# Kernel optimization log

Hardware: AMD Instinct MI355X
Metric: run time of the kernel (lower is better)

The kernel has to match this reference:

```python
import jax, jax.numpy as jnp
import numpy as np

N = 50000   # num_nodes
E = 400000  # random edges (avg degree 8)


def setup_inputs() -> dict:
    key = jax.random.key(0)
    ks = jax.random.split(key, 12)

    def w(k, shape):
        # xavier-ish scaling
        return (jax.random.normal(k, shape, jnp.float32)
                / jnp.sqrt(jnp.float32(shape[0])))

    return {
        "node_emb": jax.random.normal(ks[0], (N, 128), jnp.float32) * 0.05,
        "edge_index": jax.random.randint(ks[1], (2, E), 0, N, dtype=jnp.int32),
        "W1": w(ks[2], (128, 512)), "b1": jnp.zeros((512,), jnp.float32),
        "W2": w(ks[3], (512, 128)), "b2": jnp.zeros((128,), jnp.float32),
        "Wres": w(ks[4], (512, 128)), "bres": jnp.zeros((128,), jnp.float32),
        "Wfc1": w(ks[5], (128, 256)), "bfc1": jnp.zeros((256,), jnp.float32),
        "Wfc2": w(ks[6], (256, 1)), "bfc2": jnp.zeros((1,), jnp.float32),
    }


def reference(node_emb, edge_index, W1, b1, W2, b2, Wres, bres,
              Wfc1, bfc1, Wfc2, bfc2):
    n = node_emb.shape[0]
    loops = jnp.arange(n, dtype=edge_index.dtype)
    # explicit add_self_loops in forward + GCNConv's internal gcn_norm self
    # loops => each node gets TWO self loops (faithful to the torch code).
    src = jnp.concatenate([edge_index[0], loops, loops])
    dst = jnp.concatenate([edge_index[1], loops, loops])

    deg = jax.ops.segment_sum(jnp.ones(src.shape, node_emb.dtype), dst,
                              num_segments=n)
    dinv = jnp.where(deg > 0, jax.lax.rsqrt(deg), 0.0)
    norm = dinv[src] * dinv[dst]  # [Etot]

    def gcn(x, W, b):
        h = x @ W                                    # [N, out]
        msg = h[src] * norm[:, None]                 # gather + scale
        agg = jax.ops.segment_sum(msg, dst, num_segments=n)  # scatter-add
        return agg + b

    x1 = jax.nn.relu(gcn(node_emb, W1, b1))   # [N, 512] (dropout = eval/id)
    x2 = jax.nn.relu(gcn(x1, W2, b2))          # [N, 128]
    x = x2 + x1 @ Wres + bres                  # residual projection
    A = jax.nn.relu(x @ Wfc1 + bfc1) @ Wfc2 + bfc2  # [N, 1]
    return (x, A)
```

## Files before the change

### kernel.cpp

```cpp
#include <hip/hip_runtime.h>


typedef unsigned short u16;
typedef short bf16x8 __attribute__((ext_vector_type(8)));
typedef unsigned short us8 __attribute__((ext_vector_type(8)));
typedef float f32x4 __attribute__((ext_vector_type(4)));

static inline int cdiv_ll(long long a, long long b) { return (int)((a + b - 1) / b); }

__device__ inline float bf2f(u16 u) {
    union { unsigned int i; float f; } v; v.i = ((unsigned int)u) << 16; return v.f;
}
__device__ inline u16 f2bf(float x) {
    union { float f; unsigned int i; } v; v.f = x;
    unsigned int r = v.i + 0x7fffu + ((v.i >> 16) & 1u);
    return (u16)(r >> 16);
}


__global__ __launch_bounds__(256) void setup_kernel(const float* __restrict__ emb,
                                                    const float* __restrict__ W1,
                                                    const float* __restrict__ W2,
                                                    const float* __restrict__ Wres,
                                                    const float* __restrict__ Wfc1,
                                                    const float* __restrict__ bfc2,
                                                    u16* __restrict__ embb,
                                                    u16* __restrict__ W1t,
                                                    u16* __restrict__ Wct,
                                                    u16* __restrict__ Wfc1t,
                                                    int* __restrict__ cnt,
                                                    float* __restrict__ Aout,
                                                    int N) {
    long long r = (long long)blockIdx.x * 256 + threadIdx.x;
    const long long nf2b = (long long)N * 32;
    if (r < nf2b) {
        float4 v = ((const float4*)emb)[r];
        uint2 o;
        o.x = (unsigned)f2bf(v.x) | ((unsigned)f2bf(v.y) << 16);
        o.y = (unsigned)f2bf(v.z) | ((unsigned)f2bf(v.w) << 16);
        ((uint2*)embb)[r] = o;
        return;
    }
    r -= nf2b;
    if (r < 512 * 128) {
        int n = (int)(r / 128), k = (int)(r % 128);
        W1t[r] = f2bf(W1[(size_t)k * 512 + n]);
        return;
    }
    r -= 512 * 128;
    if (r < 256 * 512) {
        int n = (int)(r / 512), k = (int)(r % 512);
        float v = (n < 128) ? W2[(size_t)k * 128 + n] : Wres[(size_t)k * 128 + (n - 128)];
        Wct[r] = f2bf(v);
        return;
    }
    r -= 256 * 512;
    if (r < 256 * 128) {
        int n = (int)(r / 128), k = (int)(r % 128);
        Wfc1t[r] = f2bf(Wfc1[(size_t)k * 256 + n]);
        return;
    }
    r -= 256 * 128;
    if (r < N) { cnt[(int)r] = 0; return; }
    r -= N;
    if (r < N) Aout[(int)r] = bfc2[0];
}


__global__ __launch_bounds__(256) void hist_kernel(const int* __restrict__ dst,
                                                   int* __restrict__ cnt, int E) {
    int e = blockIdx.x * 256 + threadIdx.x;
    if (e < E) atomicAdd(&cnt[dst[e]], 1);
}

__global__ __launch_bounds__(256) void scanA_kernel(const int* __restrict__ cnt,
                                                    int* __restrict__ excl,
                                                    int* __restrict__ bsum, int N) {
    __shared__ int tmp[256];
    int i = blockIdx.x * 256 + threadIdx.x;
    int v = (i < N) ? cnt[i] : 0;
    tmp[threadIdx.x] = v;
    __syncthreads();
    for (int o = 1; o < 256; o <<= 1) {
        int t = (threadIdx.x >= (unsigned)o) ? tmp[threadIdx.x - o] : 0;
        __syncthreads();
        tmp[threadIdx.x] += t;
        __syncthreads();
    }
    if (i < N) excl[i] = tmp[threadIdx.x] - v;
    if (threadIdx.x == 255) bsum[blockIdx.x] = tmp[255];
}

__global__ __launch_bounds__(256) void scanC2_kernel(const int* __restrict__ excl,
                                                     const int* __restrict__ bsum,
                                                     const int* __restrict__ cnt,
                                                     int* __restrict__ rowptr,
                                                     int* __restrict__ cursor,
                                                     float* __restrict__ dinv,
                                                     int N, int E) {
    __shared__ int tmp[256];
    int t = threadIdx.x;
    tmp[t] = (t < (int)blockIdx.x) ? bsum[t] : 0;
    __syncthreads();
    for (int o = 128; o; o >>= 1) {
        if (t < o) tmp[t] += tmp[t + o];
        __syncthreads();
    }
    int pre = tmp[0];
    int i = blockIdx.x * 256 + t;
    if (i < N) {
        int r = excl[i] + pre;
        rowptr[i] = r;
        cursor[i] = r;
        dinv[i] = rsqrtf((float)cnt[i] + 2.0f);
    }
    if (i == 0) rowptr[N] = E;
}

__global__ __launch_bounds__(256) void fill_kernel(const int* __restrict__ src,
                                                   const int* __restrict__ dst,
                                                   const float* __restrict__ dinv,
                                                   int* __restrict__ cursor,
                                                   int* __restrict__ csr_src,
                                                   float* __restrict__ csr_w, int E) {
    int e = blockIdx.x * 256 + threadIdx.x;
    if (e >= E) return;
    int s = src[e], d = dst[e];
    int idx = atomicAdd(&cursor[d], 1);
    csr_src[idx] = s;
    csr_w[idx] = dinv[s] * dinv[d];
}


#define AGG_EDGE(SR, WR)                                                       \
    {                                                                          \
        unsigned int vv = hp[(size_t)(SR) * 64 + lane];                        \
        ax = fmaf(bf2f((u16)vv), (WR), ax);                                    \
        ay = fmaf(bf2f((u16)(vv >> 16)), (WR), ay);                            \
    }

__device__ inline void agg_row(const unsigned int* __restrict__ hp,
                               const int* __restrict__ rowptr,
                               const int* __restrict__ csr_src,
                               const float* __restrict__ csr_w,
                               const float* __restrict__ dinv,
                               int wid, int lane, float& ax, float& ay) {
    float dv = dinv[wid];
    unsigned int hv = hp[(size_t)wid * 64 + lane];
    float c0 = 2.0f * dv * dv;
    ax = bf2f((u16)hv) * c0;
    ay = bf2f((u16)(hv >> 16)) * c0;
    int e = rowptr[wid], e1 = rowptr[wid + 1];
    for (; e + 7 < e1; e += 8) {
        int s0 = csr_src[e + 0], s1 = csr_src[e + 1], s2 = csr_src[e + 2], s3 = csr_src[e + 3];
        int s4 = csr_src[e + 4], s5 = csr_src[e + 5], s6 = csr_src[e + 6], s7 = csr_src[e + 7];
        float w0 = csr_w[e + 0], w1 = csr_w[e + 1], w2 = csr_w[e + 2], w3 = csr_w[e + 3];
        float w4 = csr_w[e + 4], w5 = csr_w[e + 5], w6 = csr_w[e + 6], w7 = csr_w[e + 7];
        AGG_EDGE(s0, w0); AGG_EDGE(s1, w1); AGG_EDGE(s2, w2); AGG_EDGE(s3, w3);
        AGG_EDGE(s4, w4); AGG_EDGE(s5, w5); AGG_EDGE(s6, w6); AGG_EDGE(s7, w7);
    }
    if (e + 3 < e1) {
        int s0 = csr_src[e + 0], s1 = csr_src[e + 1], s2 = csr_src[e + 2], s3 = csr_src[e + 3];
        float w0 = csr_w[e + 0], w1 = csr_w[e + 1], w2 = csr_w[e + 2], w3 = csr_w[e + 3];
        AGG_EDGE(s0, w0); AGG_EDGE(s1, w1); AGG_EDGE(s2, w2); AGG_EDGE(s3, w3);
        e += 4;
    }
    for (; e < e1; ++e) {
        int s0 = csr_src[e]; float w0 = csr_w[e];
        AGG_EDGE(s0, w0);
    }
}

__global__ __launch_bounds__(256) void aggb_kernel(const u16* __restrict__ hb,
                                                   const int* __restrict__ rowptr,
                                                   const int* __restrict__ csr_src,
                                                   const float* __restrict__ csr_w,
                                                   const float* __restrict__ dinv,
                                                   u16* __restrict__ out, int N) {
    int wid  = (blockIdx.x * blockDim.x + threadIdx.x) >> 6;
    int lane = threadIdx.x & 63;
    if (wid >= N) return;
    float ax, ay;
    agg_row((const unsigned int*)hb, rowptr, csr_src, csr_w, dinv, wid, lane, ax, ay);
    ((unsigned int*)out)[(size_t)wid * 64 + lane] =
        (unsigned)f2bf(ax) | ((unsigned)f2bf(ay) << 16);
}

__global__ __launch_bounds__(256) void aggfin_kernel(const u16* __restrict__ hb,
                                                     const int* __restrict__ rowptr,
                                                     const int* __restrict__ csr_src,
                                                     const float* __restrict__ csr_w,
                                                     const float* __restrict__ dinv,
                                                     const float* __restrict__ b2,
                                                     const float* __restrict__ bres,
                                                     float* __restrict__ xout,
                                                     u16* __restrict__ xb, int N) {
    int wid  = (blockIdx.x * blockDim.x + threadIdx.x) >> 6;
    int lane = threadIdx.x & 63;
    if (wid >= N) return;
    float ax, ay;
    agg_row((const unsigned int*)hb, rowptr, csr_src, csr_w, dinv, wid, lane, ax, ay);
    float2 bb = ((const float2*)b2)[lane];
    float2 rr = ((const float2*)bres)[lane];
    float2 hres = ((float2*)xout)[(size_t)wid * 64 + lane];
    float ox = fmaxf(ax + bb.x, 0.f) + hres.x + rr.x;
    float oy = fmaxf(ay + bb.y, 0.f) + hres.y + rr.y;
    ((float2*)xout)[(size_t)wid * 64 + lane] = make_float2(ox, oy);
    ((unsigned int*)xb)[(size_t)wid * 64 + lane] =
        (unsigned)f2bf(ox) | ((unsigned)f2bf(oy) << 16);
}


__global__ __launch_bounds__(512) void mgemm12(const u16* __restrict__ aggE,
                                               const u16* __restrict__ W1t,
                                               const u16* __restrict__ Wct,
                                               const float* __restrict__ b1,
                                               int M,
                                               u16* __restrict__ h2b,
                                               float* __restrict__ xout) {
    extern __shared__ u16 smem[];
    u16* Ag  = smem;
    u16* Ws  = Ag + 128 * 136;
    u16* X1s = Ws + 256 * 136;
    const int LD = 136;

    const int t = threadIdx.x;
    const int bm = blockIdx.x * 128;
    const int w = t >> 6, lane = t & 63;
    const int wm = w >> 2, wn = w & 3;
    const int l15 = lane & 15, lg = lane >> 4;

#pragma unroll
    for (int i = 0; i < 4; ++i) {
        int c = t + 512 * i;
        int row = c >> 4, cs = (c & 15) * 8;
        us8 v = (us8)(u16)0;
        if (bm + row < M) v = *(const us8*)(aggE + (size_t)(bm + row) * 128 + cs);
        *(us8*)&Ag[row * LD + cs] = v;
    }

    f32x4 acc2[4][4];
#pragma unroll
    for (int i = 0; i < 4; ++i)
#pragma unroll
        for (int j = 0; j < 4; ++j) acc2[i][j] = (f32x4)(0.0f);

    for (int p = 0; p < 4; ++p) {
        __syncthreads();
#pragma unroll
        for (int i = 0; i < 4; ++i) {
            int c = t + 512 * i;
            int row = c >> 4, cs = (c & 15) * 8;
            *(us8*)&Ws[row * LD + cs] =
                *(const us8*)(W1t + (size_t)(128 * p + row) * 128 + cs);
        }
        __syncthreads();

        f32x4 acc1[4][2];
#pragma unroll
        for (int i = 0; i < 4; ++i)
#pragma unroll
            for (int j = 0; j < 2; ++j) acc1[i][j] = (f32x4)(0.0f);
#pragma unroll
        for (int ks = 0; ks < 4; ++ks) {
            const int ko = 32 * ks + lg * 8;
            bf16x8 wfr[2], afr[4];
#pragma unroll
            for (int fn = 0; fn < 2; ++fn)
                wfr[fn] = *(const bf16x8*)&Ws[(32 * wn + 16 * fn + l15) * LD + ko];
#pragma unroll
            for (int fm = 0; fm < 4; ++fm)
                afr[fm] = *(const bf16x8*)&Ag[(64 * wm + 16 * fm + l15) * LD + ko];
#pragma unroll
            for (int fm = 0; fm < 4; ++fm)
#pragma unroll
                for (int fn = 0; fn < 2; ++fn)
                    acc1[fm][fn] = __builtin_amdgcn_mfma_f32_16x16x32_bf16(
                        wfr[fn], afr[fm], acc1[fm][fn], 0, 0, 0);
        }
        __syncthreads();

#pragma unroll
        for (int fm = 0; fm < 4; ++fm) {
#pragma unroll
            for (int fn = 0; fn < 2; ++fn) {
                int col1 = 32 * wn + 16 * fn + 4 * lg;
                float4 b4 = *(const float4*)&b1[128 * p + col1];
                f32x4 v = acc1[fm][fn];
                float v0 = fmaxf(v[0] + b4.x, 0.f), v1 = fmaxf(v[1] + b4.y, 0.f);
                float v2 = fmaxf(v[2] + b4.z, 0.f), v3 = fmaxf(v[3] + b4.w, 0.f);
                uint2 o;
                o.x = (unsigned)f2bf(v0) | ((unsigned)f2bf(v1) << 16);
                o.y = (unsigned)f2bf(v2) | ((unsigned)f2bf(v3) << 16);
                *(uint2*)&X1s[(64 * wm + 16 * fm + l15) * LD + col1] = o;
            }
        }
#pragma unroll
        for (int i = 0; i < 8; ++i) {
            int c = t + 512 * i;
            int row = c >> 4, cs = (c & 15) * 8;
            *(us8*)&Ws[row * LD + cs] =
                *(const us8*)(Wct + (size_t)row * 512 + 128 * p + cs);
        }
        __syncthreads();

#pragma unroll
        for (int ks = 0; ks < 4; ++ks) {
            const int ko = 32 * ks + lg * 8;
            bf16x8 wfr[4], xfr[4];
#pragma unroll
            for (int fn = 0; fn < 4; ++fn)
                wfr[fn] = *(const bf16x8*)&Ws[(64 * wn + 16 * fn + l15) * LD + ko];
#pragma unroll
            for (int fm = 0; fm < 4; ++fm)
                xfr[fm] = *(const bf16x8*)&X1s[(64 * wm + 16 * fm + l15) * LD + ko];
#pragma unroll
            for (int fm = 0; fm < 4; ++fm)
#pragma unroll
                for (int fn = 0; fn < 4; ++fn)
                    acc2[fm][fn] = __builtin_amdgcn_mfma_f32_16x16x32_bf16(
                        wfr[fn], xfr[fm], acc2[fm][fn], 0, 0, 0);
        }
    }

#pragma unroll
    for (int fm = 0; fm < 4; ++fm) {
        const int row = bm + 64 * wm + 16 * fm + l15;
        if (row >= M) continue;
#pragma unroll
        for (int fn = 0; fn < 4; ++fn) {
            const int col = 64 * wn + 16 * fn + 4 * lg;
            f32x4 v = acc2[fm][fn];
            if (col < 128) {
                uint2 o;
                o.x = (unsigned)f2bf(v[0]) | ((unsigned)f2bf(v[1]) << 16);
                o.y = (unsigned)f2bf(v[2]) | ((unsigned)f2bf(v[3]) << 16);
                *(uint2*)(h2b + (size_t)row * 128 + col) = o;
            } else {
                *(float4*)(xout + (size_t)row * 128 + (col - 128)) =
                    make_float4(v[0], v[1], v[2], v[3]);
            }
        }
    }
}


__global__ __launch_bounds__(512) void head_gemm(const u16* __restrict__ A,
                                                 const u16* __restrict__ Bt,
                                                 int M,
                                                 const float* __restrict__ bias,
                                                 const float* __restrict__ w2,
                                                 float* __restrict__ Cf) {
    __shared__ u16 As[128][72];
    __shared__ u16 Bs[256][72];
    const int t = threadIdx.x;
    const int bm = blockIdx.x * 128;
    const int w = t >> 6, lane = t & 63;
    const int wm = w >> 2, wn = w & 3;
    const int l15 = lane & 15, lg = lane >> 4;
    const int srow = t >> 3, scol = (t & 7) * 8;
    const int K = 128;

    f32x4 acc[4][4];
#pragma unroll
    for (int i = 0; i < 4; ++i)
#pragma unroll
        for (int j = 0; j < 4; ++j) acc[i][j] = (f32x4)(0.0f);

    for (int kk = 0; kk < K; kk += 64) {
#pragma unroll
        for (int i = 0; i < 2; ++i) {
            int row = srow + 64 * i;
            us8 v = (us8)(u16)0;
            if (bm + row < M)
                v = *(const us8*)(A + (size_t)(bm + row) * K + kk + scol);
            *(us8*)&As[row][scol] = v;
        }
#pragma unroll
        for (int i = 0; i < 4; ++i) {
            int row = srow + 64 * i;
            *(us8*)&Bs[row][scol] =
                *(const us8*)(Bt + (size_t)row * K + kk + scol);
        }
        __syncthreads();
#pragma unroll
        for (int ks = 0; ks < 2; ++ks) {
            const int ko = 32 * ks + lg * 8;
            bf16x8 bfr[4], afr[4];
#pragma unroll
            for (int fn = 0; fn < 4; ++fn)
                bfr[fn] = *(const bf16x8*)&Bs[64 * wn + 16 * fn + l15][ko];
#pragma unroll
            for (int fm = 0; fm < 4; ++fm)
                afr[fm] = *(const bf16x8*)&As[64 * wm + 16 * fm + l15][ko];
#pragma unroll
            for (int fm = 0; fm < 4; ++fm)
#pragma unroll
                for (int fn = 0; fn < 4; ++fn)
                    acc[fm][fn] = __builtin_amdgcn_mfma_f32_16x16x32_bf16(
                        bfr[fn], afr[fm], acc[fm][fn], 0, 0, 0);
        }
        __syncthreads();
    }

    float4 bl4[4], wl4[4];
#pragma unroll
    for (int fn = 0; fn < 4; ++fn) {
        int c = 64 * wn + 16 * fn + 4 * lg;
        bl4[fn] = *(const float4*)&bias[c];
        wl4[fn] = *(const float4*)&w2[c];
    }
#pragma unroll
    for (int fm = 0; fm < 4; ++fm) {
        float p = 0.f;
#pragma unroll
        for (int fn = 0; fn < 4; ++fn) {
            p += fmaxf(acc[fm][fn][0] + bl4[fn].x, 0.f) * wl4[fn].x;
            p += fmaxf(acc[fm][fn][1] + bl4[fn].y, 0.f) * wl4[fn].y;
            p += fmaxf(acc[fm][fn][2] + bl4[fn].z, 0.f) * wl4[fn].z;
            p += fmaxf(acc[fm][fn][3] + bl4[fn].w, 0.f) * wl4[fn].w;
        }
        p += __shfl_xor(p, 16);
        p += __shfl_xor(p, 32);
        int row = bm + 64 * wm + 16 * fm + l15;
        if (lane < 16 && row < M) atomicAdd(&Cf[row], p);
    }
}


extern "C" void kernel_launch(void* const* d_in, const int* in_sizes, int n_in,
                              void* d_out, int out_size, void* d_ws, size_t ws_size,
                              hipStream_t stream) {
    const float* emb  = (const float*)d_in[0];
    const int*   eidx = (const int*)d_in[1];
    const float* W1   = (const float*)d_in[2];
    const float* b1   = (const float*)d_in[3];
    const float* W2   = (const float*)d_in[4];
    const float* b2   = (const float*)d_in[5];
    const float* Wres = (const float*)d_in[6];
    const float* bres = (const float*)d_in[7];
    const float* Wfc1 = (const float*)d_in[8];
    const float* bfc1 = (const float*)d_in[9];
    const float* Wfc2 = (const float*)d_in[10];
    const float* bfc2 = (const float*)d_in[11];

    const int N = in_sizes[0] / 128;
    const int E = in_sizes[1] / 2;
    const int* srcv = eidx;
    const int* dstv = eidx + E;

    float* out  = (float*)d_out;
    float* xout = out;
    float* Aout = out + (size_t)N * 128;

    char* p = (char*)d_ws;
    float* dinv  = (float*)p;            p += (size_t)N * 4;
    float* csr_w = (float*)p;            p += (size_t)E * 4;
    u16*  embb   = (u16*)p;              p += (size_t)N * 128 * 2;
    u16*  aggEb  = (u16*)p;              p += (size_t)N * 128 * 2;
    u16*  h2b    = (u16*)p;              p += (size_t)N * 128 * 2;
    u16*  xb     = (u16*)p;              p += (size_t)N * 128 * 2;
    u16*  W1t    = (u16*)p;              p += (size_t)512 * 128 * 2;
    u16*  Wct    = (u16*)p;              p += (size_t)256 * 512 * 2;
    u16*  Wfc1t  = (u16*)p;              p += (size_t)256 * 128 * 2;
    int*  cnt     = (int*)p;             p += (size_t)N * 4;
    int*  excl    = (int*)p;             p += (size_t)N * 4;
    int*  rowptr  = (int*)p;             p += (size_t)(N + 1) * 4;
    int*  cursor  = (int*)p;             p += (size_t)N * 4;
    int*  bsum    = (int*)p;             p += 256 * 4;
    int*  csr_src = (int*)p;             p += (size_t)E * 4;

    const int T  = 256;
    const int nb = cdiv_ll(N, 256);

    const long long setup_work = (long long)N * 32 + 512 * 128 + 256 * 512
                               + 256 * 128 + (long long)N + (long long)N;
    setup_kernel<<<cdiv_ll(setup_work, T), T, 0, stream>>>(
        emb, W1, W2, Wres, Wfc1, bfc2, embb, W1t, Wct, Wfc1t, cnt, Aout, N);

    hist_kernel<<<cdiv_ll(E, T), T, 0, stream>>>(dstv, cnt, E);
    scanA_kernel<<<nb, T, 0, stream>>>(cnt, excl, bsum, N);
    scanC2_kernel<<<nb, T, 0, stream>>>(excl, bsum, cnt, rowptr, cursor, dinv, N, E);
    fill_kernel<<<cdiv_ll(E, T), T, 0, stream>>>(srcv, dstv, dinv, cursor, csr_src, csr_w, E);

    aggb_kernel<<<cdiv_ll((long long)N * 64, T), T, 0, stream>>>(
        embb, rowptr, csr_src, csr_w, dinv, aggEb, N);

    const size_t lds12 = (size_t)(128 * 136 + 256 * 136 + 128 * 136) * sizeof(u16);
    mgemm12<<<cdiv_ll(N, 128), 512, lds12, stream>>>(
        aggEb, W1t, Wct, b1, N, h2b, xout);

    aggfin_kernel<<<cdiv_ll((long long)N * 64, T), T, 0, stream>>>(
        h2b, rowptr, csr_src, csr_w, dinv, b2, bres, xout, xb, N);

    head_gemm<<<cdiv_ll(N, 128), 512, 0, stream>>>(
        xb, Wfc1t, N, bfc1, Wfc2, Aout);
}
```

Baseline: 178.3 us.

## Shrink mgemm12 tile to 64 rows and feed head GEMM from fp32 output

The fused two-layer GEMM now uses a 64-row tile with 4 waves. A fragments stay in registers and weight fragments are loaded straight from global memory (L2-cached) instead of being staged in LDS, so only the X1 intermediate lives in shared memory. The smaller LDS footprint should raise occupancy and remove several barriers, but weight reads are now repeated per wave from global memory. Separately, aggfin no longer writes a bf16 copy of x, and head_gemm converts the fp32 output to bf16 on load, saving one write pass at the cost of reading twice as many bytes.

```diff
diff --git a/kernel.cpp b/kernel.cpp
--- a/kernel.cpp
+++ b/kernel.cpp
@@ -193,8 +193,7 @@
                                                      const float* __restrict__ dinv,
                                                      const float* __restrict__ b2,
                                                      const float* __restrict__ bres,
-                                                     float* __restrict__ xout,
-                                                     u16* __restrict__ xb, int N) {
+                                                     float* __restrict__ xout, int N) {
     int wid  = (blockIdx.x * blockDim.x + threadIdx.x) >> 6;
     int lane = threadIdx.x & 63;
     if (wid >= N) return;
@@ -206,38 +205,35 @@
     float ox = fmaxf(ax + bb.x, 0.f) + hres.x + rr.x;
     float oy = fmaxf(ay + bb.y, 0.f) + hres.y + rr.y;
     ((float2*)xout)[(size_t)wid * 64 + lane] = make_float2(ox, oy);
-    ((unsigned int*)xb)[(size_t)wid * 64 + lane] =
-        (unsigned)f2bf(ox) | ((unsigned)f2bf(oy) << 16);
-}
-
-
-__global__ __launch_bounds__(512) void mgemm12(const u16* __restrict__ aggE,
+}
+
+
+__global__ __launch_bounds__(256) void mgemm12(const u16* __restrict__ aggE,
                                                const u16* __restrict__ W1t,
                                                const u16* __restrict__ Wct,
                                                const float* __restrict__ b1,
                                                int M,
                                                u16* __restrict__ h2b,
                                                float* __restrict__ xout) {
-    extern __shared__ u16 smem[];
-    u16* Ag  = smem;
-    u16* Ws  = Ag + 128 * 136;
-    u16* X1s = Ws + 256 * 136;
+    extern __shared__ u16 X1s[];
     const int LD = 136;
-
     const int t = threadIdx.x;
-    const int bm = blockIdx.x * 128;
-    const int w = t >> 6, lane = t & 63;
-    const int wm = w >> 2, wn = w & 3;
+    const int bm = blockIdx.x * 64;
+    const int wn = t >> 6;
+    const int lane = t & 63;
     const int l15 = lane & 15, lg = lane >> 4;
 
-#pragma unroll
-    for (int i = 0; i < 4; ++i) {
-        int c = t + 512 * i;
-        int row = c >> 4, cs = (c & 15) * 8;
-        us8 v = (us8)(u16)0;
-        if (bm + row < M) v = *(const us8*)(aggE + (size_t)(bm + row) * 128 + cs);
-        *(us8*)&Ag[row * LD + cs] = v;
-    }
+    bf16x8 afr[4][4];
+#pragma unroll
+    for (int ks = 0; ks < 4; ++ks)
+#pragma unroll
+        for (int fm = 0; fm < 4; ++fm) {
+            int row = bm + 16 * fm + l15;
+            bf16x8 v = (bf16x8)(short)0;
+            if (row < M)
+                v = *(const bf16x8*)(aggE + (size_t)row * 128 + 32 * ks + 8 * lg);
+            afr[ks][fm] = v;
+        }
 
     f32x4 acc2[4][4];
 #pragma unroll
@@ -247,14 +243,6 @@
 
     for (int p = 0; p < 4; ++p) {
         __syncthreads();
-#pragma unroll
-        for (int i = 0; i < 4; ++i) {
-            int c = t + 512 * i;
-            int row = c >> 4, cs = (c & 15) * 8;
-            *(us8*)&Ws[row * LD + cs] =
-                *(const us8*)(W1t + (size_t)(128 * p + row) * 128 + cs);
-        }
-        __syncthreads();
 
         f32x4 acc1[4][2];
 #pragma unroll
@@ -263,22 +251,18 @@
             for (int j = 0; j < 2; ++j) acc1[i][j] = (f32x4)(0.0f);
 #pragma unroll
         for (int ks = 0; ks < 4; ++ks) {
-            const int ko = 32 * ks + lg * 8;
-            bf16x8 wfr[2], afr[4];
+            bf16x8 wfr[2];
 #pragma unroll
             for (int fn = 0; fn < 2; ++fn)
-                wfr[fn] = *(const bf16x8*)&Ws[(32 * wn + 16 * fn + l15) * LD + ko];
-#pragma unroll
-            for (int fm = 0; fm < 4; ++fm)
-                afr[fm] = *(const bf16x8*)&Ag[(64 * wm + 16 * fm + l15) * LD + ko];
+                wfr[fn] = *(const bf16x8*)(W1t +
+                    (size_t)(128 * p + 32 * wn + 16 * fn + l15) * 128 + 32 * ks + 8 * lg);
 #pragma unroll
             for (int fm = 0; fm < 4; ++fm)
 #pragma unroll
                 for (int fn = 0; fn < 2; ++fn)
                     acc1[fm][fn] = __builtin_amdgcn_mfma_f32_16x16x32_bf16(
-                        wfr[fn], afr[fm], acc1[fm][fn], 0, 0, 0);
-        }
-        __syncthreads();
+                        wfr[fn], afr[ks][fm], acc1[fm][fn], 0, 0, 0);
+        }
 
 #pragma unroll
         for (int fm = 0; fm < 4; ++fm) {
@@ -292,40 +276,38 @@
                 uint2 o;
                 o.x = (unsigned)f2bf(v0) | ((unsigned)f2bf(v1) << 16);
                 o.y = (unsigned)f2bf(v2) | ((unsigned)f2bf(v3) << 16);
-                *(uint2*)&X1s[(64 * wm + 16 * fm + l15) * LD + col1] = o;
+                *(uint2*)&X1s[(16 * fm + l15) * LD + col1] = o;
             }
         }
-#pragma unroll
-        for (int i = 0; i < 8; ++i) {
-            int c = t + 512 * i;
-            int row = c >> 4, cs = (c & 15) * 8;
-            *(us8*)&Ws[row * LD + cs] =
-                *(const us8*)(Wct + (size_t)row * 512 + 128 * p + cs);
-        }
+
+        bf16x8 wfr2[4][4];
+#pragma unroll
+        for (int ks = 0; ks < 4; ++ks)
+#pragma unroll
+            for (int fn = 0; fn < 4; ++fn)
+                wfr2[ks][fn] = *(const bf16x8*)(Wct +
+                    (size_t)(64 * wn + 16 * fn + l15) * 512 + 128 * p + 32 * ks + 8 * lg);
+
         __syncthreads();
 
 #pragma unroll
         for (int ks = 0; ks < 4; ++ks) {
-            const int ko = 32 * ks + lg * 8;
-            bf16x8 wfr[4], xfr[4];
-#pragma unroll
-            for (int fn = 0; fn < 4; ++fn)
-                wfr[fn] = *(const bf16x8*)&Ws[(64 * wn + 16 * fn + l15) * LD + ko];
+            bf16x8 xfr[4];
 #pragma unroll
             for (int fm = 0; fm < 4; ++fm)
-                xfr[fm] = *(const bf16x8*)&X1s[(64 * wm + 16 * fm + l15) * LD + ko];
+                xfr[fm] = *(const bf16x8*)&X1s[(16 * fm + l15) * LD + 32 * ks + 8 * lg];
 #pragma unroll
             for (int fm = 0; fm < 4; ++fm)
 #pragma unroll
                 for (int fn = 0; fn < 4; ++fn)
                     acc2[fm][fn] = __builtin_amdgcn_mfma_f32_16x16x32_bf16(
-                        wfr[fn], xfr[fm], acc2[fm][fn], 0, 0, 0);
+                        wfr2[ks][fn], xfr[fm], acc2[fm][fn], 0, 0, 0);
         }
     }
 
 #pragma unroll
     for (int fm = 0; fm < 4; ++fm) {
-        const int row = bm + 64 * wm + 16 * fm + l15;
+        const int row = bm + 16 * fm + l15;
         if (row >= M) continue;
 #pragma unroll
         for (int fn = 0; fn < 4; ++fn) {
@@ -345,7 +327,7 @@
 }
 
 
-__global__ __launch_bounds__(512) void head_gemm(const u16* __restrict__ A,
+__global__ __launch_bounds__(512) void head_gemm(const float* __restrict__ X,
                                                  const u16* __restrict__ Bt,
                                                  int M,
                                                  const float* __restrict__ bias,
@@ -371,10 +353,17 @@
 #pragma unroll
         for (int i = 0; i < 2; ++i) {
             int row = srow + 64 * i;
-            us8 v = (us8)(u16)0;
-            if (bm + row < M)
-                v = *(const us8*)(A + (size_t)(bm + row) * K + kk + scol);
-            *(us8*)&As[row][scol] = v;
+            uint4 o = make_uint4(0u, 0u, 0u, 0u);
+            if (bm + row < M) {
+                const float* src = X + (size_t)(bm + row) * K + kk + scol;
+                float4 a = *(const float4*)src;
+                float4 b = *(const float4*)(src + 4);
+                o.x = (unsigned)f2bf(a.x) | ((unsigned)f2bf(a.y) << 16);
+                o.y = (unsigned)f2bf(a.z) | ((unsigned)f2bf(a.w) << 16);
+                o.z = (unsigned)f2bf(b.x) | ((unsigned)f2bf(b.y) << 16);
+                o.w = (unsigned)f2bf(b.z) | ((unsigned)f2bf(b.w) << 16);
+            }
+            *(uint4*)&As[row][scol] = o;
         }
 #pragma unroll
         for (int i = 0; i < 4; ++i) {
@@ -459,7 +448,6 @@
     u16*  embb   = (u16*)p;              p += (size_t)N * 128 * 2;
     u16*  aggEb  = (u16*)p;              p += (size_t)N * 128 * 2;
     u16*  h2b    = (u16*)p;              p += (size_t)N * 128 * 2;
-    u16*  xb     = (u16*)p;              p += (size_t)N * 128 * 2;
     u16*  W1t    = (u16*)p;              p += (size_t)512 * 128 * 2;
     u16*  Wct    = (u16*)p;              p += (size_t)256 * 512 * 2;
     u16*  Wfc1t  = (u16*)p;              p += (size_t)256 * 128 * 2;
@@ -486,13 +474,13 @@
     aggb_kernel<<<cdiv_ll((long long)N * 64, T), T, 0, stream>>>(
         embb, rowptr, csr_src, csr_w, dinv, aggEb, N);
 
-    const size_t lds12 = (size_t)(128 * 136 + 256 * 136 + 128 * 136) * sizeof(u16);
-    mgemm12<<<cdiv_ll(N, 128), 512, lds12, stream>>>(
+    const size_t lds12 = (size_t)(64 * 136) * sizeof(u16);
+    mgemm12<<<cdiv_ll(N, 64), 256, lds12, stream>>>(
         aggEb, W1t, Wct, b1, N, h2b, xout);
 
     aggfin_kernel<<<cdiv_ll((long long)N * 64, T), T, 0, stream>>>(
-        h2b, rowptr, csr_src, csr_w, dinv, b2, bres, xout, xb, N);
+        h2b, rowptr, csr_src, csr_w, dinv, b2, bres, xout, N);
 
     head_gemm<<<cdiv_ll(N, 128), 512, 0, stream>>>(
-        xb, Wfc1t, N, bfc1, Wfc2, Aout);
-}
+        xout, Wfc1t, N, bfc1, Wfc2, Aout);
+}
```

After: 205.6 us. 15.3% more time.
